# Kernel tuning notes

Hardware: AMD Instinct MI355X
Metric: run time of the kernel (lower is better)

## Reference

```python
import jax, jax.numpy as jnp
import numpy as np


def setup_inputs() -> dict:
    key = jax.random.key(0)
    ks = jax.random.split(key, 8)
    B, C, H, W = 4, 256, 64, 64
    C8 = C // 8
    x = jax.random.normal(ks[0], (B, C, H, W), dtype=jnp.float32)
    # 1x1 conv weights as (out_ch, in_ch) matrices + biases
    Wq = jax.random.normal(ks[1], (C8, C), dtype=jnp.float32) * (1.0 / np.sqrt(C))
    bq = jnp.zeros((C8,), dtype=jnp.float32)
    Wk = jax.random.normal(ks[2], (C8, C), dtype=jnp.float32) * (1.0 / np.sqrt(C))
    bk = jnp.zeros((C8,), dtype=jnp.float32)
    Wv = jax.random.normal(ks[3], (C, C), dtype=jnp.float32) * (1.0 / np.sqrt(C))
    bv = jnp.zeros((C,), dtype=jnp.float32)
    gamma = jax.random.normal(ks[4], (1,), dtype=jnp.float32) * 0.1
    return {"x": x, "Wq": Wq, "bq": bq, "Wk": Wk, "bk": bk, "Wv": Wv, "bv": bv, "gamma": gamma}


def reference(x, Wq, bq, Wk, bk, Wv, bv, gamma):
    B, C, H, W = x.shape
    N = H * W
    xf = x.reshape(B, C, N)  # (B, C, N)
    # 1x1 convs == per-pixel channel matmuls
    q = jnp.einsum('oc,bcn->bon', Wq, xf) + bq[None, :, None]  # (B, C8, N)
    k = jnp.einsum('oc,bcn->bon', Wk, xf) + bk[None, :, None]  # (B, C8, N)
    v = jnp.einsum('oc,bcn->bon', Wv, xf) + bv[None, :, None]  # (B, C, N)
    energy = jnp.einsum('bcn,bcm->bnm', q, k)  # (B, N, N)
    attention = jax.nn.softmax(energy, axis=-1)
    # out[b,c,n] = sum_m v[b,c,m] * attention[b,n,m]
    out = jnp.einsum('bcm,bnm->bcn', v, attention)
    out = out.reshape(B, C, H, W)
    return gamma * out + x
```

## Files before the change

kernel.cpp:

```cpp
#include <hip/hip_runtime.h>
#include <hip/hip_bf16.h>
#include <cstddef>
#include <cstdint>

#define CCH 256
#define DQK 32
#define NPX 4096
#define BQK 256
#define BM  64
#define NB  4
#define NW  16

typedef __attribute__((ext_vector_type(8))) short bf16x8;
typedef __attribute__((ext_vector_type(4))) float f32x4;
typedef __attribute__((ext_vector_type(4))) unsigned int u32x4;

#if __has_builtin(__builtin_amdgcn_exp2f)
#define EXP2F(x) __builtin_amdgcn_exp2f(x)
#else
#define EXP2F(x) exp2f(x)
#endif

__device__ inline unsigned short f2bf(float f) {
    unsigned u = __builtin_bit_cast(unsigned, f);
    u += 0x7FFFu + ((u >> 16) & 1u);
    return (unsigned short)(u >> 16);
}
__device__ inline float bf2f(unsigned short h) {
    unsigned u = (unsigned)h << 16;
    return __builtin_bit_cast(float, u);
}
__device__ inline unsigned pkbf(float a, float b) {
    __hip_bfloat162 h = __float22bfloat162_rn(make_float2(a, b));
    unsigned u;
    __builtin_memcpy(&u, &h, 4);
    return u;
}

__global__ __launch_bounds__(256) void convert_kernel(
    const float* __restrict__ Wq, const float* __restrict__ bq,
    const float* __restrict__ Wk, const float* __restrict__ bk,
    const float* __restrict__ Wv, const float* __restrict__ bv,
    unsigned short* __restrict__ Wb, float* __restrict__ bb)
{
    const float LOG2E = 1.4426950408889634f;
    const int o = blockIdx.x;
    const int c = threadIdx.x;
    float v;
    if (o < 32)       v = Wq[o * CCH + c] * LOG2E;
    else if (o < 64)  v = Wk[(o - 32) * CCH + c];
    else              v = Wv[(o - 64) * CCH + c];
    Wb[o * CCH + c] = f2bf(v);
    if (c == 0)
        bb[o] = (o < 32) ? bq[o] * LOG2E : (o < 64) ? bk[o - 32] : bv[o - 64];
}

__global__ __launch_bounds__(512) void proj_mfma(
    const float* __restrict__ x,
    const unsigned short* __restrict__ Wb, const float* __restrict__ bb,
    unsigned short* __restrict__ ws)
{
    __shared__ __align__(16) unsigned short xT[64][264];

    const int tid  = threadIdx.x;
    const int lane = tid & 63;
    const int w    = tid >> 6;
    const int ln   = lane & 15;
    const int g    = lane >> 4;
    const int bid  = blockIdx.x;

    const int xcd  = bid & 7;
    const int idx  = bid >> 3;
    const int slab = xcd + 8 * (idx / 5);
    const int ocg  = idx % 5;
    const int b    = slab >> 6;
    const int pxt  = slab & 63;
    const int pxg0 = pxt * 64;

    const int mt    = w >> 1;
    const int ocrow = ocg * 64 + mt * 16 + ln;
    bf16x8 a[8];
#pragma unroll
    for (int k8 = 0; k8 < 8; ++k8)
        a[k8] = *(const bf16x8*)(Wb + (size_t)ocrow * CCH + k8 * 32 + g * 8);

    {
        const int pxl = (tid & 15) * 4;
        const int c0  = (tid >> 4) * 8;
        float4 xv[8];
#pragma unroll
        for (int cc = 0; cc < 8; ++cc)
            xv[cc] = *(const float4*)(x + ((size_t)(b * CCH + c0 + cc)) * NPX + pxg0 + pxl);
#pragma unroll
        for (int j = 0; j < 4; ++j) {
            unsigned u[4];
#pragma unroll
            for (int h = 0; h < 4; ++h) {
                const float f0 = ((const float*)&xv[2 * h])[j];
                const float f1 = ((const float*)&xv[2 * h + 1])[j];
                u[h] = pkbf(f0, f1);
            }
            *(u32x4*)&xT[pxl + j][c0] = (u32x4){u[0], u[1], u[2], u[3]};
        }
    }
    __syncthreads();

    const int nt0 = (w & 1) * 2;
    const float4 bb4 = *(const float4*)(bb + ocg * 64 + mt * 16 + g * 4);
    f32x4 acc0 = (f32x4){bb4.x, bb4.y, bb4.z, bb4.w};
    f32x4 acc1 = acc0;
#pragma unroll
    for (int k8 = 0; k8 < 8; ++k8) {
        const bf16x8 b0 = *(const bf16x8*)&xT[nt0 * 16 + ln][k8 * 32 + g * 8];
        const bf16x8 b1 = *(const bf16x8*)&xT[nt0 * 16 + 16 + ln][k8 * 32 + g * 8];
        acc0 = __builtin_amdgcn_mfma_f32_16x16x32_bf16(a[k8], b0, acc0, 0, 0, 0);
        acc1 = __builtin_amdgcn_mfma_f32_16x16x32_bf16(a[k8], b1, acc1, 0, 0, 0);
    }

    unsigned short* qT = ws;
    unsigned short* kT = ws + (size_t)NB * NPX * 32;
    unsigned short* vb = ws + (size_t)2 * NB * NPX * 32;
#pragma unroll
    for (int j = 0; j < 2; ++j) {
        const f32x4 acc = j ? acc1 : acc0;
        const int px = pxg0 + (nt0 + j) * 16 + ln;
        if (ocg == 0) {
            const unsigned lo = pkbf(acc[0], acc[1]);
            const unsigned hi = pkbf(acc[2], acc[3]);
            unsigned short* dst = (mt < 2)
                ? qT + ((size_t)b * NPX + px) * 32 + mt * 16 + g * 4
                : kT + ((size_t)b * NPX + px) * 32 + (mt - 2) * 16 + g * 4;
            *(uint2*)dst = make_uint2(lo, hi);
        } else {
            const int c_row = (ocg - 1) * 64 + mt * 16 + g * 4;
#pragma unroll
            for (int rr = 0; rr < 4; ++rr)
                vb[((size_t)(b * CCH + c_row + rr)) * NPX + px] = f2bf(acc[rr]);
        }
    }
}

__global__ __launch_bounds__(1024, 4) void attn_kernel(
    const unsigned short* __restrict__ qT, const unsigned short* __restrict__ kT,
    const unsigned short* __restrict__ vB, const float* __restrict__ x,
    const float* __restrict__ gamma, float* __restrict__ out,
    unsigned short* __restrict__ opart, float* __restrict__ mlm,
    float* __restrict__ mll, int ns)
{
    __shared__ __align__(16) unsigned short Pl[2][BQK * 64];
    __shared__ __align__(16) unsigned short Kl[2][64 * 32];
    __shared__ float scb[2][BQK];
    __shared__ int   flg[2][NW];
    __shared__ float l_lds[BQK];

    const int tid  = threadIdx.x;
    const int lane = tid & 63;
    const int w    = tid >> 6;
    const int ln   = lane & 15;
    const int g    = lane >> 4;
    const int bid  = blockIdx.x;

    const int b    = (bid & 7) >> 1;
    const int jb   = ((bid >> 3) << 1) | (bid & 1);
    const int tile = jb / ns;
    const int s    = jb - tile * ns;
    const int n0   = tile * BQK;

    const bf16x8 qf = *(const bf16x8*)(qT + ((size_t)b * NPX + n0 + w * 16 + ln) * 32 + g * 8);

    f32x4 acc[16];
#pragma unroll
    for (int qt = 0; qt < 16; ++qt) acc[qt] = (f32x4){0.f, 0.f, 0.f, 0.f};
    float mreg = -INFINITY, lreg = 0.f;

    const unsigned short* kTb = kT + (size_t)b * NPX * 32;
    const unsigned short* vb  = vB + ((size_t)b * CCH + w * 16) * NPX;
    const int kbase = s * (NPX / ns);
    const int iters = NPX / (ns * BM);
    const unsigned swz   = ((unsigned)ln & 7u) << 4;
    const unsigned myrow = (unsigned)(w * 16 + ln) * 128u;
    const float THR2 = 11.544655f;

    if (w < 4) {
        const unsigned short* ksrc = kTb + (size_t)kbase * 32 + w * 512 + lane * 8;
        __builtin_amdgcn_global_load_lds(
            (const __attribute__((address_space(1))) void*)ksrc,
            (__attribute__((address_space(3))) void*)&Kl[0][w * 512], 16, 0, 0);
    }
    asm volatile("s_waitcnt vmcnt(0)" ::: "memory");
    __syncthreads();

    for (int t = 0; t < iters; ++t) {
        const int m0 = kbase + t * BM;
        const int mnext = (t + 1 < iters) ? (m0 + BM) : m0;
        const int nbuf = (t + 1) & 1;

        if (w < 4) {
            const unsigned short* ksrc = kTb + (size_t)mnext * 32 + w * 512 + lane * 8;
            __builtin_amdgcn_global_load_lds(
                (const __attribute__((address_space(1))) void*)ksrc,
                (__attribute__((address_space(3))) void*)&Kl[nbuf][w * 512], 16, 0, 0);
        }

        const unsigned short* kl = &Kl[t & 1][0];
        f32x4 e[4];
#pragma unroll
        for (int s4 = 0; s4 < 4; ++s4) {
            const bf16x8 ka = *(const bf16x8*)(kl + (s4 * 16 + ln) * 32 + g * 8);
            e[s4] = __builtin_amdgcn_mfma_f32_16x16x32_bf16(
                        ka, qf, (f32x4){0.f, 0.f, 0.f, 0.f}, 0, 0, 0);
        }

        float lm = -INFINITY;
#pragma unroll
        for (int s4 = 0; s4 < 4; ++s4)
#pragma unroll
            for (int rr = 0; rr < 4; ++rr) lm = fmaxf(lm, e[s4][rr]);
        lm = fmaxf(lm, __shfl_xor(lm, 16));
        lm = fmaxf(lm, __shfl_xor(lm, 32));
        const float mnew = (lm <= mreg + THR2) ? mreg : lm;
        const float sc   = EXP2F(mreg - mnew);
        float ps = 0.f;
#pragma unroll
        for (int s4 = 0; s4 < 4; ++s4)
#pragma unroll
            for (int rr = 0; rr < 4; ++rr) {
                const float p = EXP2F(e[s4][rr] - mnew);
                e[s4][rr] = p;
                ps += p;
            }
        ps += __shfl_xor(ps, 16);
        ps += __shfl_xor(ps, 32);
        lreg = lreg * sc + ps;
        mreg = mnew;

        const int bw = t & 1;
        char* const pwb = (char*)&Pl[bw][0];
#pragma unroll
        for (int s4 = 0; s4 < 4; ++s4) {
            uint2 pk;
            pk.x = pkbf(e[s4][0], e[s4][1]);
            pk.y = pkbf(e[s4][2], e[s4][3]);
            *(uint2*)(pwb + myrow + (((unsigned)(s4 * 32 + g * 8)) ^ swz)) = pk;
        }
        if (g == 0) scb[bw][w * 16 + ln] = sc;
        const int allsk = __all(sc == 1.0f);
        if (lane == 0) flg[bw][w] = allsk;

        const unsigned short* vrow = vb + (size_t)ln * NPX + m0 + g * 8;
        bf16x8 va0 = *(const bf16x8*)(vrow);
        bf16x8 va1 = *(const bf16x8*)(vrow + 32);

        asm volatile("s_waitcnt vmcnt(2) lgkmcnt(0)" ::: "memory");
        __builtin_amdgcn_s_barrier();

        int sk = flg[bw][0];
#pragma unroll
        for (int i = 1; i < NW; ++i) sk &= flg[bw][i];
        if (!sk) {
#pragma unroll
            for (int qt = 0; qt < 16; ++qt) {
                const float scq = scb[bw][qt * 16 + ln];
#pragma unroll
                for (int rr = 0; rr < 4; ++rr) acc[qt][rr] *= scq;
            }
        }
#pragma unroll
        for (int qt = 0; qt < 16; ++qt) {
            const unsigned rb = (unsigned)(qt * 16 + ln) * 128u;
            const bf16x8 pf0 = *(const bf16x8*)(pwb + rb + (((unsigned)(g * 16))      ^ swz));
            const bf16x8 pf1 = *(const bf16x8*)(pwb + rb + (((unsigned)(64 + g * 16)) ^ swz));
            acc[qt] = __builtin_amdgcn_mfma_f32_16x16x32_bf16(va0, pf0, acc[qt], 0, 0, 0);
            acc[qt] = __builtin_amdgcn_mfma_f32_16x16x32_bf16(va1, pf1, acc[qt], 0, 0, 0);
        }
    }

    if (opart) {
        const size_t sb = (size_t)(s * NB + b);
#pragma unroll
        for (int qt = 0; qt < 16; ++qt) {
            const size_t c0 = sb * CCH + w * 16 + g * 4;
#pragma unroll
            for (int rr = 0; rr < 4; ++rr)
                opart[(c0 + rr) * NPX + n0 + qt * 16 + ln] = f2bf(acc[qt][rr]);
        }
        if (g == 0) {
            mlm[sb * NPX + n0 + w * 16 + ln] = mreg;
            mll[sb * NPX + n0 + w * 16 + ln] = lreg;
        }
    } else {
        if (g == 0) l_lds[w * 16 + ln] = lreg;
        __syncthreads();
        const float gm = gamma[0];
#pragma unroll
        for (int qt = 0; qt < 16; ++qt) {
            const float iv = 1.f / l_lds[qt * 16 + ln];
            const size_t c0 = (size_t)b * CCH + w * 16 + g * 4;
#pragma unroll
            for (int rr = 0; rr < 4; ++rr) {
                const size_t idx = (c0 + rr) * NPX + n0 + qt * 16 + ln;
                out[idx] = gm * acc[qt][rr] * iv + x[idx];
            }
        }
    }
}

__global__ __launch_bounds__(256) void combine_kernel(
    const unsigned short* __restrict__ opart,
    const float* __restrict__ mlm, const float* __restrict__ mll,
    const float* __restrict__ x, const float* __restrict__ gamma,
    float* __restrict__ out, int ns)
{
    const int idx = blockIdx.x * 256 + threadIdx.x;
    const int bc  = idx >> 9;
    const int b   = bc / CCH;
    const int c   = bc - b * CCH;
    const int n0  = (idx & 511) * 8;

    float M[8];
#pragma unroll
    for (int i = 0; i < 8; ++i) M[i] = -INFINITY;
    for (int s = 0; s < ns; ++s) {
        const float* mp = mlm + ((size_t)(s * NB + b)) * NPX + n0;
#pragma unroll
        for (int i = 0; i < 8; ++i) M[i] = fmaxf(M[i], mp[i]);
    }

    float L[8], O[8];
#pragma unroll
    for (int i = 0; i < 8; ++i) { L[i] = 0.f; O[i] = 0.f; }
    for (int s = 0; s < ns; ++s) {
        const size_t sb = (size_t)(s * NB + b);
        const float* mp = mlm + sb * NPX + n0;
        const float* lp = mll + sb * NPX + n0;
        const bf16x8 v8 = *(const bf16x8*)(opart + (sb * CCH + c) * NPX + n0);
#pragma unroll
        for (int i = 0; i < 8; ++i) {
            const float wgt = EXP2F(mp[i] - M[i]);
            L[i] += wgt * lp[i];
            O[i] += wgt * bf2f((unsigned short)v8[i]);
        }
    }

    const float gm = gamma[0];
    const size_t xo = (size_t)bc * NPX + n0;
    float4 r0, r1;
    const float4 x0 = *(const float4*)(x + xo);
    const float4 x1 = *(const float4*)(x + xo + 4);
    r0.x = gm * O[0] / L[0] + x0.x;  r0.y = gm * O[1] / L[1] + x0.y;
    r0.z = gm * O[2] / L[2] + x0.z;  r0.w = gm * O[3] / L[3] + x0.w;
    r1.x = gm * O[4] / L[4] + x1.x;  r1.y = gm * O[5] / L[5] + x1.y;
    r1.z = gm * O[6] / L[6] + x1.z;  r1.w = gm * O[7] / L[7] + x1.w;
    *(float4*)(out + xo)     = r0;
    *(float4*)(out + xo + 4) = r1;
}

extern "C" void kernel_launch(void* const* d_in, const int* in_sizes, int n_in,
                              void* d_out, int out_size, void* d_ws, size_t ws_size,
                              hipStream_t stream)
{
    const float* x  = (const float*)d_in[0];
    const float* Wq = (const float*)d_in[1];
    const float* bq = (const float*)d_in[2];
    const float* Wk = (const float*)d_in[3];
    const float* bk = (const float*)d_in[4];
    const float* Wv = (const float*)d_in[5];
    const float* bv = (const float*)d_in[6];
    const float* gm = (const float*)d_in[7];
    float* out = (float*)d_out;
    unsigned short* ws = (unsigned short*)d_ws;

    const size_t WB_U16 = 320 * CCH;
    const size_t BB_U16 = 320 * 2;
    const size_t qkvU   = (size_t)2 * NB * NPX * 32 + (size_t)NB * CCH * NPX;
    const size_t qkvB   = (qkvU + WB_U16 + BB_U16) * 2;
    const size_t partB  = (size_t)NB * CCH * NPX * 2;
    const size_t mlB    = (size_t)2 * NB * NPX * 4;
    int ns = 1;
    if      (ws_size >= qkvB + 4 * (partB + mlB)) ns = 4;
    else if (ws_size >= qkvB + 2 * (partB + mlB)) ns = 2;

    unsigned short* Wb = ws + qkvU;
    float*          bb = (float*)(ws + qkvU + WB_U16);

    convert_kernel<<<320, 256, 0, stream>>>(Wq, bq, Wk, bk, Wv, bv, Wb, bb);

    proj_mfma<<<1280, 512, 0, stream>>>(x, Wb, bb, ws);

    const unsigned short* qT = ws;
    const unsigned short* kT = ws + (size_t)NB * NPX * 32;
    const unsigned short* vB = ws + (size_t)2 * NB * NPX * 32;

    const int ablocks = NB * (NPX / BQK) * ns;

    if (ns > 1) {
        unsigned short* opart = ws + qkvU + WB_U16 + BB_U16;
        float* mlm = (float*)(opart + (size_t)ns * NB * CCH * NPX);
        float* mll = mlm + (size_t)ns * NB * NPX;

        attn_kernel<<<ablocks, 1024, 0, stream>>>(qT, kT, vB, x, gm, out,
                                                  opart, mlm, mll, ns);

        const int cblocks = (NB * CCH * (NPX / 8)) / 256;
        combine_kernel<<<cblocks, 256, 0, stream>>>(opart, mlm, mll, x, gm, out, ns);
    } else {
        attn_kernel<<<ablocks, 1024, 0, stream>>>(qT, kT, vB, x, gm, out,
                                                  nullptr, nullptr, nullptr, 1);
    }
}
```

Before: 92.73 us.

## Stage V tiles in LDS and use 32x32 MFMA 2x2 tiling for PV

V tiles are now double-buffered in shared memory with global_load_lds, replacing per-wave direct global loads. The PV product is retiled so each wave computes a 64x64 (query x channel) block with 32x32x16 MFMAs, reusing P and V fragments across a 2x2 register tile. The intent is fewer LDS reads of P per MFMA and better MFMA efficiency. It costs an extra 64KB of LDS, which may lower occupancy, and it adds a full vmcnt(0) wait before the barrier. The output layout mapping is adjusted to match the 32x32 accumulator format.

```diff
diff --git a/kernel.cpp b/kernel.cpp
--- a/kernel.cpp
+++ b/kernel.cpp
@@ -13,6 +13,7 @@
 
 typedef __attribute__((ext_vector_type(8))) short bf16x8;
 typedef __attribute__((ext_vector_type(4))) float f32x4;
+typedef __attribute__((ext_vector_type(16))) float f32x16;
 typedef __attribute__((ext_vector_type(4))) unsigned int u32x4;
 
 #if __has_builtin(__builtin_amdgcn_exp2f)
@@ -148,6 +149,7 @@
     float* __restrict__ mll, int ns)
 {
     __shared__ __align__(16) unsigned short Pl[2][BQK * 64];
+    __shared__ __align__(16) unsigned short Vl[2][CCH * 64];
     __shared__ __align__(16) unsigned short Kl[2][64 * 32];
     __shared__ float scb[2][BQK];
     __shared__ int   flg[2][NW];
@@ -158,6 +160,8 @@
     const int w    = tid >> 6;
     const int ln   = lane & 15;
     const int g    = lane >> 4;
+    const int l32  = lane & 31;
+    const int h32  = lane >> 5;
     const int bid  = blockIdx.x;
 
     const int b    = (bid & 7) >> 1;
@@ -166,26 +170,41 @@
     const int s    = jb - tile * ns;
     const int n0   = tile * BQK;
 
+    const int qg = w & 3;
+    const int cg = w >> 2;
+
     const bf16x8 qf = *(const bf16x8*)(qT + ((size_t)b * NPX + n0 + w * 16 + ln) * 32 + g * 8);
 
-    f32x4 acc[16];
-#pragma unroll
-    for (int qt = 0; qt < 16; ++qt) acc[qt] = (f32x4){0.f, 0.f, 0.f, 0.f};
+    f32x16 acc2[2][2];
+#pragma unroll
+    for (int a0 = 0; a0 < 2; ++a0)
+#pragma unroll
+        for (int a1 = 0; a1 < 2; ++a1)
+#pragma unroll
+            for (int i = 0; i < 16; ++i) acc2[a0][a1][i] = 0.f;
     float mreg = -INFINITY, lreg = 0.f;
 
     const unsigned short* kTb = kT + (size_t)b * NPX * 32;
-    const unsigned short* vb  = vB + ((size_t)b * CCH + w * 16) * NPX;
+    const unsigned short* vBb = vB + (size_t)b * CCH * NPX;
     const int kbase = s * (NPX / ns);
     const int iters = NPX / (ns * BM);
-    const unsigned swz   = ((unsigned)ln & 7u) << 4;
+    const unsigned swz   = ((unsigned)lane & 7u) << 4;
     const unsigned myrow = (unsigned)(w * 16 + ln) * 128u;
     const float THR2 = 11.544655f;
+    const int vko = ((lane & 7) ^ ((lane >> 3) & 7)) * 8;
 
     if (w < 4) {
         const unsigned short* ksrc = kTb + (size_t)kbase * 32 + w * 512 + lane * 8;
         __builtin_amdgcn_global_load_lds(
             (const __attribute__((address_space(1))) void*)ksrc,
             (__attribute__((address_space(3))) void*)&Kl[0][w * 512], 16, 0, 0);
+    }
+#pragma unroll
+    for (int i = 0; i < 2; ++i) {
+        const unsigned short* vsrc = vBb + (size_t)(w * 16 + i * 8 + (lane >> 3)) * NPX + kbase + vko;
+        __builtin_amdgcn_global_load_lds(
+            (const __attribute__((address_space(1))) void*)vsrc,
+            (__attribute__((address_space(3))) void*)&Vl[0][(w * 16 + i * 8) * 64], 16, 0, 0);
     }
     asm volatile("s_waitcnt vmcnt(0)" ::: "memory");
     __syncthreads();
@@ -247,43 +266,59 @@
         const int allsk = __all(sc == 1.0f);
         if (lane == 0) flg[bw][w] = allsk;
 
-        const unsigned short* vrow = vb + (size_t)ln * NPX + m0 + g * 8;
-        bf16x8 va0 = *(const bf16x8*)(vrow);
-        bf16x8 va1 = *(const bf16x8*)(vrow + 32);
-
-        asm volatile("s_waitcnt vmcnt(2) lgkmcnt(0)" ::: "memory");
+        asm volatile("s_waitcnt vmcnt(0) lgkmcnt(0)" ::: "memory");
         __builtin_amdgcn_s_barrier();
+
+#pragma unroll
+        for (int i = 0; i < 2; ++i) {
+            const unsigned short* vsrc = vBb + (size_t)(w * 16 + i * 8 + (lane >> 3)) * NPX + mnext + vko;
+            __builtin_amdgcn_global_load_lds(
+                (const __attribute__((address_space(1))) void*)vsrc,
+                (__attribute__((address_space(3))) void*)&Vl[nbuf][(w * 16 + i * 8) * 64], 16, 0, 0);
+        }
 
         int sk = flg[bw][0];
 #pragma unroll
         for (int i = 1; i < NW; ++i) sk &= flg[bw][i];
         if (!sk) {
 #pragma unroll
-            for (int qt = 0; qt < 16; ++qt) {
-                const float scq = scb[bw][qt * 16 + ln];
-#pragma unroll
-                for (int rr = 0; rr < 4; ++rr) acc[qt][rr] *= scq;
+            for (int qt2 = 0; qt2 < 2; ++qt2) {
+                const float scq = scb[bw][qg * 64 + qt2 * 32 + l32];
+#pragma unroll
+                for (int ct2 = 0; ct2 < 2; ++ct2)
+#pragma unroll
+                    for (int rr = 0; rr < 16; ++rr) acc2[qt2][ct2][rr] *= scq;
             }
         }
-#pragma unroll
-        for (int qt = 0; qt < 16; ++qt) {
-            const unsigned rb = (unsigned)(qt * 16 + ln) * 128u;
-            const bf16x8 pf0 = *(const bf16x8*)(pwb + rb + (((unsigned)(g * 16))      ^ swz));
-            const bf16x8 pf1 = *(const bf16x8*)(pwb + rb + (((unsigned)(64 + g * 16)) ^ swz));
-            acc[qt] = __builtin_amdgcn_mfma_f32_16x16x32_bf16(va0, pf0, acc[qt], 0, 0, 0);
-            acc[qt] = __builtin_amdgcn_mfma_f32_16x16x32_bf16(va1, pf1, acc[qt], 0, 0, 0);
+
+        const char* vl = (const char*)&Vl[t & 1][0];
+        const char* pB = (const char*)&Pl[bw][0];
+#pragma unroll
+        for (int kc = 0; kc < 4; ++kc) {
+            const unsigned ko = (unsigned)(kc * 32 + (h32 << 4));
+            const bf16x8 pb0 = *(const bf16x8*)(pB + (qg * 64 + l32) * 128      + (ko ^ swz));
+            const bf16x8 pb1 = *(const bf16x8*)(pB + (qg * 64 + 32 + l32) * 128 + (ko ^ swz));
+            const bf16x8 va0 = *(const bf16x8*)(vl + (cg * 64 + l32) * 128      + (ko ^ swz));
+            const bf16x8 va1 = *(const bf16x8*)(vl + (cg * 64 + 32 + l32) * 128 + (ko ^ swz));
+            acc2[0][0] = __builtin_amdgcn_mfma_f32_32x32x16_bf16(va0, pb0, acc2[0][0], 0, 0, 0);
+            acc2[0][1] = __builtin_amdgcn_mfma_f32_32x32x16_bf16(va1, pb0, acc2[0][1], 0, 0, 0);
+            acc2[1][0] = __builtin_amdgcn_mfma_f32_32x32x16_bf16(va0, pb1, acc2[1][0], 0, 0, 0);
+            acc2[1][1] = __builtin_amdgcn_mfma_f32_32x32x16_bf16(va1, pb1, acc2[1][1], 0, 0, 0);
         }
     }
 
     if (opart) {
         const size_t sb = (size_t)(s * NB + b);
 #pragma unroll
-        for (int qt = 0; qt < 16; ++qt) {
-            const size_t c0 = sb * CCH + w * 16 + g * 4;
-#pragma unroll
-            for (int rr = 0; rr < 4; ++rr)
-                opart[(c0 + rr) * NPX + n0 + qt * 16 + ln] = f2bf(acc[qt][rr]);
-        }
+        for (int qt2 = 0; qt2 < 2; ++qt2)
+#pragma unroll
+            for (int ct2 = 0; ct2 < 2; ++ct2)
+#pragma unroll
+                for (int rr = 0; rr < 16; ++rr) {
+                    const int crow = cg * 64 + ct2 * 32 + (rr & 3) + 8 * (rr >> 2) + 4 * h32;
+                    opart[(sb * CCH + crow) * NPX + n0 + qg * 64 + qt2 * 32 + l32]
+                        = f2bf(acc2[qt2][ct2][rr]);
+                }
         if (g == 0) {
             mlm[sb * NPX + n0 + w * 16 + ln] = mreg;
             mll[sb * NPX + n0 + w * 16 + ln] = lreg;
@@ -293,14 +328,17 @@
         __syncthreads();
         const float gm = gamma[0];
 #pragma unroll
-        for (int qt = 0; qt < 16; ++qt) {
-            const float iv = 1.f / l_lds[qt * 16 + ln];
-            const size_t c0 = (size_t)b * CCH + w * 16 + g * 4;
-#pragma unroll
-            for (int rr = 0; rr < 4; ++rr) {
-                const size_t idx = (c0 + rr) * NPX + n0 + qt * 16 + ln;
-                out[idx] = gm * acc[qt][rr] * iv + x[idx];
-            }
+        for (int qt2 = 0; qt2 < 2; ++qt2) {
+            const float iv = 1.f / l_lds[qg * 64 + qt2 * 32 + l32];
+#pragma unroll
+            for (int ct2 = 0; ct2 < 2; ++ct2)
+#pragma unroll
+                for (int rr = 0; rr < 16; ++rr) {
+                    const int crow = cg * 64 + ct2 * 32 + (rr & 3) + 8 * (rr >> 2) + 4 * h32;
+                    const size_t idx = ((size_t)b * CCH + crow) * NPX
+                                     + n0 + qg * 64 + qt2 * 32 + l32;
+                    out[idx] = gm * acc2[qt2][ct2][rr] * iv + x[idx];
+                }
         }
     }
 }
```

After: 95.25 us. 2.7% more time.
